# Optimization experiments

Hardware: AMD Instinct MI355X
Metric: run time of the kernel (lower is better)

Reference implementation:

```python
import jax, jax.numpy as jnp
import numpy as np

B, T, I, H, O = 8192, 1024, 7, 100, 1


def setup_inputs() -> dict:
    key = jax.random.key(0)
    ks = jax.random.split(key, 7)
    s = 1.0 / np.sqrt(H)  # PyTorch default init bound for RNN/Linear(H)
    return {
        "x": jax.random.normal(ks[0], (B, T, I), dtype=jnp.float32),
        "W_ih": jax.random.uniform(ks[1], (H, I), jnp.float32, -s, s),
        "W_hh": jax.random.uniform(ks[2], (H, H), jnp.float32, -s, s),
        "b_ih": jax.random.uniform(ks[3], (H,), jnp.float32, -s, s),
        "b_hh": jax.random.uniform(ks[4], (H,), jnp.float32, -s, s),
        "W_fc": jax.random.uniform(ks[5], (O, H), jnp.float32, -s, s),
        "b_fc": jax.random.uniform(ks[6], (O,), jnp.float32, -s, s),
    }


def reference(x, W_ih, W_hh, b_ih, b_hh, W_fc, b_fc):
    # Precompute the input projection for all timesteps in one GEMM:
    # x_proj[b,t,h] = x[b,t,:] @ W_ih^T + b_ih + b_hh  (both biases folded in)
    x_proj = jnp.einsum('bti,hi->bth', x, W_ih) + b_ih + b_hh  # [B,T,H]

    def step(h, xt):
        # h_t = relu(x_t W_ih^T + b_ih + h_{t-1} W_hh^T + b_hh)
        h_new = jax.nn.relu(xt + h @ W_hh.T)
        return h_new, None

    h0 = jnp.zeros((x.shape[0], W_hh.shape[0]), dtype=x.dtype)  # [B,H]
    hT, _ = jax.lax.scan(step, h0, jnp.swapaxes(x_proj, 0, 1))  # scan over T

    # fc applied to last timestep only: out[:, -1, :] @ W_fc^T + b_fc
    return hT @ W_fc.T + b_fc  # [B,O]
```

## Files before the change

### kernel.cpp

```cpp
#include <hip/hip_runtime.h>


typedef _Float16 half8 __attribute__((ext_vector_type(8)));
typedef float f32x4 __attribute__((ext_vector_type(4)));
typedef unsigned u32x4 __attribute__((ext_vector_type(4)));

static __device__ __forceinline__ unsigned pkrtz(float a, float b) {
    return __builtin_bit_cast(unsigned, __builtin_amdgcn_cvt_pkrtz(a, b));
}

static __device__ __forceinline__ f32x4 ld4(const float* p) {
    typedef f32x4 __attribute__((aligned(4))) f32x4a;
    return *(const f32x4a*)p;
}

__global__ __launch_bounds__(64, 1)
void rnn_wave(const float* __restrict__ x,
              const float* __restrict__ W_ih,
              const float* __restrict__ W_hh,
              const float* __restrict__ b_ih,
              const float* __restrict__ b_hh,
              const float* __restrict__ W_fc,
              const float* __restrict__ b_fc,
              float* __restrict__ out) {
    const int l  = threadIdx.x;
    const int lm = l & 15;
    const int q  = l >> 4;
    const bool q1 = (q == 1);

    half8 w[7][4];
#pragma unroll
    for (int ti = 0; ti < 7; ++ti) {
        const int np = 16 * ti + lm;
#pragma unroll
        for (int kt = 0; kt < 4; ++kt) {
            half8 hw;
#pragma unroll
            for (int jj = 0; jj < 8; ++jj) {
                float v = 0.f;
                if (np < 100) {
                    if (jj < 4) {
                        int p = 16 * kt + 4 * q + jj;
                        if (p < 100) v = W_hh[np * 100 + p];
                    } else if (kt < 3) {
                        int p = 16 * (kt + 4) + 4 * q + (jj - 4);
                        if (p < 100) v = W_hh[np * 100 + p];
                    } else {
                        if (q == 0)      v = W_ih[np * 7 + (jj - 4)];
                        else if (q == 1) v = (jj < 7) ? W_ih[np * 7 + jj]
                                             : (b_ih[np] + b_hh[np]);
                    }
                }
                hw[jj] = (_Float16)v;
            }
            w[ti][kt] = hw;
        }
    }

    const float* xr = x + (size_t)(blockIdx.x * 16 + lm) * 7168;
    const int xo = q1 ? 3 : 0;

    const u32x4 zz = {0u, 0u, 0u, 0u};
    const half8 hz = __builtin_bit_cast(half8, zz);

    half8 hf[4];
    {
        f32x4 v = ld4(xr + xo);
        float x0 = q1 ? v.y : v.x, x1 = q1 ? v.z : v.y;
        float x2 = q1 ? v.w : v.z, x3 = q1 ? 1.0f : v.w;
        hf[0] = hz; hf[1] = hz; hf[2] = hz;
        u32x4 h3 = {0u, 0u, pkrtz(x0, x1), pkrtz(x2, x3)};
        hf[3] = __builtin_bit_cast(half8, h3);
    }

    float xv[4][4];
#pragma unroll
    for (int s = 1; s <= 4; ++s) {
        f32x4 v = ld4(xr + s * 7 + xo);
        xv[s & 3][0] = q1 ? v.y : v.x;
        xv[s & 3][1] = q1 ? v.z : v.y;
        xv[s & 3][2] = q1 ? v.w : v.z;
        xv[s & 3][3] = q1 ? 1.0f : v.w;
    }

    const f32x4 kZ = {0.f, 0.f, 0.f, 0.f};
    f32x4 acc[7];

    for (int tb = 0; tb < 1024; tb += 4) {
#pragma unroll
        for (int u = 0; u < 4; ++u) {
            const int t = tb + u;

#pragma unroll
            for (int kt = 0; kt < 4; ++kt) {
                const int order[7] = {0, 4, 1, 5, 2, 6, 3};
#pragma unroll
                for (int oi = 0; oi < 7; ++oi) {
                    const int ti = order[oi];
                    acc[ti] = __builtin_amdgcn_mfma_f32_16x16x32_f16(
                        w[ti][kt], hf[kt], (kt == 0) ? kZ : acc[ti], 0, 0, 0);
                }
            }

            const int s = (u + 1) & 3;
#pragma unroll
            for (int kt = 0; kt < 3; ++kt) {
                u32x4 d;
                d.x = pkrtz(acc[kt][0],     acc[kt][1]);
                d.y = pkrtz(acc[kt][2],     acc[kt][3]);
                d.z = pkrtz(acc[kt + 4][0], acc[kt + 4][1]);
                d.w = pkrtz(acc[kt + 4][2], acc[kt + 4][3]);
                hf[kt] = __builtin_elementwise_max(__builtin_bit_cast(half8, d), hz);
            }
            {
                u32x4 d;
                d.x = pkrtz(fmaxf(acc[3][0], 0.f), fmaxf(acc[3][1], 0.f));
                d.y = pkrtz(fmaxf(acc[3][2], 0.f), fmaxf(acc[3][3], 0.f));
                d.z = pkrtz(xv[s][0], xv[s][1]);
                d.w = pkrtz(xv[s][2], xv[s][3]);
                hf[3] = __builtin_bit_cast(half8, d);
            }

            int tn = t + 5; if (tn > 1023) tn = 1023;
            {
                f32x4 v = ld4(xr + tn * 7 + xo);
                xv[s][0] = q1 ? v.y : v.x;
                xv[s][1] = q1 ? v.z : v.y;
                xv[s][2] = q1 ? v.w : v.z;
                xv[s][3] = q1 ? 1.0f : v.w;
            }
        }
    }

    float sum = 0.f;
#pragma unroll
    for (int ti = 0; ti < 7; ++ti) {
#pragma unroll
        for (int r = 0; r < 4; ++r) {
            const int np = 16 * ti + 4 * q + r;
            const float wf = (np < 100) ? W_fc[np] : 0.f;
            sum += wf * fmaxf(acc[ti][r], 0.f);
        }
    }
    sum += __shfl_xor(sum, 16, 64);
    sum += __shfl_xor(sum, 32, 64);
    if (q == 0) out[blockIdx.x * 16 + lm] = sum + b_fc[0];
}

extern "C" void kernel_launch(void* const* d_in, const int* in_sizes, int n_in,
                              void* d_out, int out_size, void* d_ws, size_t ws_size,
                              hipStream_t stream) {
    const float* x    = (const float*)d_in[0];
    const float* W_ih = (const float*)d_in[1];
    const float* W_hh = (const float*)d_in[2];
    const float* b_ih = (const float*)d_in[3];
    const float* b_hh = (const float*)d_in[4];
    const float* W_fc = (const float*)d_in[5];
    const float* b_fc = (const float*)d_in[6];
    float* out = (float*)d_out;

    rnn_wave<<<dim3(512), dim3(64), 0, stream>>>(x, W_ih, W_hh, b_ih, b_hh, W_fc, b_fc, out);
}
```

Baseline: 670.8 us.

## Interleave hidden-state packing with MFMAs using sched_group_barrier ordering

```diff
diff --git a/kernel.cpp b/kernel.cpp
--- a/kernel.cpp
+++ b/kernel.cpp
@@ -13,6 +13,8 @@
     typedef f32x4 __attribute__((aligned(4))) f32x4a;
     return *(const f32x4a*)p;
 }
+
+#define SGB(mask, n) __builtin_amdgcn_sched_group_barrier(mask, n, 0)
 
 __global__ __launch_bounds__(64, 1)
 void rnn_wave(const float* __restrict__ x,
@@ -63,72 +65,101 @@
     const u32x4 zz = {0u, 0u, 0u, 0u};
     const half8 hz = __builtin_bit_cast(half8, zz);
 
-    half8 hf[4];
-    {
-        f32x4 v = ld4(xr + xo);
-        float x0 = q1 ? v.y : v.x, x1 = q1 ? v.z : v.y;
-        float x2 = q1 ? v.w : v.z, x3 = q1 ? 1.0f : v.w;
-        hf[0] = hz; hf[1] = hz; hf[2] = hz;
-        u32x4 h3 = {0u, 0u, pkrtz(x0, x1), pkrtz(x2, x3)};
-        hf[3] = __builtin_bit_cast(half8, h3);
-    }
-
-    float xv[4][4];
+    f32x4 xv[4];
 #pragma unroll
-    for (int s = 1; s <= 4; ++s) {
-        f32x4 v = ld4(xr + s * 7 + xo);
-        xv[s & 3][0] = q1 ? v.y : v.x;
-        xv[s & 3][1] = q1 ? v.z : v.y;
-        xv[s & 3][2] = q1 ? v.w : v.z;
-        xv[s & 3][3] = q1 ? 1.0f : v.w;
-    }
+    for (int s = 0; s < 4; ++s) xv[s] = ld4(xr + s * 7 + xo);
 
     const f32x4 kZ = {0.f, 0.f, 0.f, 0.f};
     f32x4 acc[7];
+#pragma unroll
+    for (int i = 0; i < 7; ++i) acc[i] = kZ;
+    half8 hf[4];
 
     for (int tb = 0; tb < 1024; tb += 4) {
 #pragma unroll
         for (int u = 0; u < 4; ++u) {
             const int t = tb + u;
 
+            {
+                u32x4 d;
+                d.x = pkrtz(acc[0][0], acc[0][1]);
+                d.y = pkrtz(acc[0][2], acc[0][3]);
+                d.z = pkrtz(acc[4][0], acc[4][1]);
+                d.w = pkrtz(acc[4][2], acc[4][3]);
+                hf[0] = __builtin_elementwise_max(__builtin_bit_cast(half8, d), hz);
+            }
+            SGB(0x2, 8);
+            acc[0] = __builtin_amdgcn_mfma_f32_16x16x32_f16(w[0][0], hf[0], kZ, 0, 0, 0);
+            acc[4] = __builtin_amdgcn_mfma_f32_16x16x32_f16(w[4][0], hf[0], kZ, 0, 0, 0);
+            SGB(0x8, 2);
+            {
+                u32x4 d;
+                d.x = pkrtz(acc[1][0], acc[1][1]);
+                d.y = pkrtz(acc[1][2], acc[1][3]);
+                d.z = pkrtz(acc[5][0], acc[5][1]);
+                d.w = pkrtz(acc[5][2], acc[5][3]);
+                hf[1] = __builtin_elementwise_max(__builtin_bit_cast(half8, d), hz);
+            }
+            SGB(0x2, 8);
+            acc[1] = __builtin_amdgcn_mfma_f32_16x16x32_f16(w[1][0], hf[0], kZ, 0, 0, 0);
+            acc[5] = __builtin_amdgcn_mfma_f32_16x16x32_f16(w[5][0], hf[0], kZ, 0, 0, 0);
+            SGB(0x8, 2);
+            {
+                u32x4 d;
+                d.x = pkrtz(acc[2][0], acc[2][1]);
+                d.y = pkrtz(acc[2][2], acc[2][3]);
+                d.z = pkrtz(acc[6][0], acc[6][1]);
+                d.w = pkrtz(acc[6][2], acc[6][3]);
+                hf[2] = __builtin_elementwise_max(__builtin_bit_cast(half8, d), hz);
+            }
+            SGB(0x2, 8);
+            acc[2] = __builtin_amdgcn_mfma_f32_16x16x32_f16(w[2][0], hf[0], kZ, 0, 0, 0);
+            acc[6] = __builtin_amdgcn_mfma_f32_16x16x32_f16(w[6][0], hf[0], kZ, 0, 0, 0);
+            SGB(0x8, 2);
+            {
+                f32x4 v = xv[u];
+                float a_ = q1 ? v.y : v.x, b_ = q1 ? v.z : v.y;
+                float c_ = q1 ? v.w : v.z, e_ = q1 ? 1.0f : v.w;
+                u32x4 d;
+                d.x = pkrtz(fmaxf(acc[3][0], 0.f), fmaxf(acc[3][1], 0.f));
+                d.y = pkrtz(fmaxf(acc[3][2], 0.f), fmaxf(acc[3][3], 0.f));
+                d.z = pkrtz(a_, b_);
+                d.w = pkrtz(c_, e_);
+                hf[3] = __builtin_bit_cast(half8, d);
+            }
+            SGB(0x2, 12);
+            acc[3] = __builtin_amdgcn_mfma_f32_16x16x32_f16(w[3][0], hf[0], kZ, 0, 0, 0);
+            SGB(0x8, 1);
+
+            acc[0] = __builtin_amdgcn_mfma_f32_16x16x32_f16(w[0][1], hf[1], acc[0], 0, 0, 0);
+            acc[1] = __builtin_amdgcn_mfma_f32_16x16x32_f16(w[1][1], hf[1], acc[1], 0, 0, 0);
+            SGB(0x8, 2);
+            {
+                int tn = t + 4; if (tn > 1023) tn = 1023;
+                xv[u] = ld4(xr + tn * 7 + xo);
+            }
+            SGB(0x20, 1);
+            acc[2] = __builtin_amdgcn_mfma_f32_16x16x32_f16(w[2][1], hf[1], acc[2], 0, 0, 0);
+            acc[3] = __builtin_amdgcn_mfma_f32_16x16x32_f16(w[3][1], hf[1], acc[3], 0, 0, 0);
+            acc[4] = __builtin_amdgcn_mfma_f32_16x16x32_f16(w[4][1], hf[1], acc[4], 0, 0, 0);
+            acc[5] = __builtin_amdgcn_mfma_f32_16x16x32_f16(w[5][1], hf[1], acc[5], 0, 0, 0);
+            acc[6] = __builtin_amdgcn_mfma_f32_16x16x32_f16(w[6][1], hf[1], acc[6], 0, 0, 0);
+            SGB(0x8, 5);
+
 #pragma unroll
-            for (int kt = 0; kt < 4; ++kt) {
+            for (int ti = 0; ti < 7; ++ti)
+                acc[ti] = __builtin_amdgcn_mfma_f32_16x16x32_f16(w[ti][2], hf[2], acc[ti], 0, 0, 0);
+            SGB(0x8, 7);
+
+            {
                 const int order[7] = {0, 4, 1, 5, 2, 6, 3};
 #pragma unroll
                 for (int oi = 0; oi < 7; ++oi) {
                     const int ti = order[oi];
-                    acc[ti] = __builtin_amdgcn_mfma_f32_16x16x32_f16(
-                        w[ti][kt], hf[kt], (kt == 0) ? kZ : acc[ti], 0, 0, 0);
+                    acc[ti] = __builtin_amdgcn_mfma_f32_16x16x32_f16(w[ti][3], hf[3], acc[ti], 0, 0, 0);
                 }
             }
-
-            const int s = (u + 1) & 3;
-#pragma unroll
-            for (int kt = 0; kt < 3; ++kt) {
-                u32x4 d;
-                d.x = pkrtz(acc[kt][0],     acc[kt][1]);
-                d.y = pkrtz(acc[kt][2],     acc[kt][3]);
-                d.z = pkrtz(acc[kt + 4][0], acc[kt + 4][1]);
-                d.w = pkrtz(acc[kt + 4][2], acc[kt + 4][3]);
-                hf[kt] = __builtin_elementwise_max(__builtin_bit_cast(half8, d), hz);
-            }
-            {
-                u32x4 d;
-                d.x = pkrtz(fmaxf(acc[3][0], 0.f), fmaxf(acc[3][1], 0.f));
-                d.y = pkrtz(fmaxf(acc[3][2], 0.f), fmaxf(acc[3][3], 0.f));
-                d.z = pkrtz(xv[s][0], xv[s][1]);
-                d.w = pkrtz(xv[s][2], xv[s][3]);
-                hf[3] = __builtin_bit_cast(half8, d);
-            }
-
-            int tn = t + 5; if (tn > 1023) tn = 1023;
-            {
-                f32x4 v = ld4(xr + tn * 7 + xo);
-                xv[s][0] = q1 ? v.y : v.x;
-                xv[s][1] = q1 ? v.z : v.y;
-                xv[s][2] = q1 ? v.w : v.z;
-                xv[s][3] = q1 ? 1.0f : v.w;
-            }
+            SGB(0x8, 7);
         }
     }
 
```

Result: faster. 647.0 us (-3.6%).

## Split MFMA accumulation into even/odd chains and interleave packing with MFMAs

Applied to the files above, without the earlier changes.

```diff
diff --git a/kernel.cpp b/kernel.cpp
--- a/kernel.cpp
+++ b/kernel.cpp
@@ -13,6 +13,23 @@
     typedef f32x4 __attribute__((aligned(4))) f32x4a;
     return *(const f32x4a*)p;
 }
+
+static __device__ __forceinline__ half8 pack_relu(f32x4 e0, f32x4 o0,
+                                                  f32x4 e1, f32x4 o1) {
+    const u32x4 zz = {0u, 0u, 0u, 0u};
+    const half8 hz = __builtin_bit_cast(half8, zz);
+    f32x4 s0 = e0 + o0;
+    f32x4 s1 = e1 + o1;
+    u32x4 d;
+    d.x = pkrtz(s0[0], s0[1]);
+    d.y = pkrtz(s0[2], s0[3]);
+    d.z = pkrtz(s1[0], s1[1]);
+    d.w = pkrtz(s1[2], s1[3]);
+    return __builtin_elementwise_max(__builtin_bit_cast(half8, d), hz);
+}
+
+#define SGB(mask, n) __builtin_amdgcn_sched_group_barrier(mask, n, 0)
+#define MFMA16(a, b, c) __builtin_amdgcn_mfma_f32_16x16x32_f16(a, b, c, 0, 0, 0)
 
 __global__ __launch_bounds__(64, 1)
 void rnn_wave(const float* __restrict__ x,
@@ -60,75 +77,79 @@
     const float* xr = x + (size_t)(blockIdx.x * 16 + lm) * 7168;
     const int xo = q1 ? 3 : 0;
 
-    const u32x4 zz = {0u, 0u, 0u, 0u};
-    const half8 hz = __builtin_bit_cast(half8, zz);
-
-    half8 hf[4];
-    {
-        f32x4 v = ld4(xr + xo);
-        float x0 = q1 ? v.y : v.x, x1 = q1 ? v.z : v.y;
-        float x2 = q1 ? v.w : v.z, x3 = q1 ? 1.0f : v.w;
-        hf[0] = hz; hf[1] = hz; hf[2] = hz;
-        u32x4 h3 = {0u, 0u, pkrtz(x0, x1), pkrtz(x2, x3)};
-        hf[3] = __builtin_bit_cast(half8, h3);
-    }
-
-    float xv[4][4];
+    f32x4 xv[4];
 #pragma unroll
-    for (int s = 1; s <= 4; ++s) {
-        f32x4 v = ld4(xr + s * 7 + xo);
-        xv[s & 3][0] = q1 ? v.y : v.x;
-        xv[s & 3][1] = q1 ? v.z : v.y;
-        xv[s & 3][2] = q1 ? v.w : v.z;
-        xv[s & 3][3] = q1 ? 1.0f : v.w;
-    }
+    for (int s = 0; s < 4; ++s) xv[s] = ld4(xr + s * 7 + xo);
 
     const f32x4 kZ = {0.f, 0.f, 0.f, 0.f};
-    f32x4 acc[7];
+    f32x4 accE[7], accO[7];
+#pragma unroll
+    for (int i = 0; i < 7; ++i) { accE[i] = kZ; accO[i] = kZ; }
+    half8 hf[4];
 
     for (int tb = 0; tb < 1024; tb += 4) {
 #pragma unroll
         for (int u = 0; u < 4; ++u) {
             const int t = tb + u;
 
-#pragma unroll
-            for (int kt = 0; kt < 4; ++kt) {
-                const int order[7] = {0, 4, 1, 5, 2, 6, 3};
-#pragma unroll
-                for (int oi = 0; oi < 7; ++oi) {
-                    const int ti = order[oi];
-                    acc[ti] = __builtin_amdgcn_mfma_f32_16x16x32_f16(
-                        w[ti][kt], hf[kt], (kt == 0) ? kZ : acc[ti], 0, 0, 0);
-                }
-            }
+            hf[0] = pack_relu(accE[0], accO[0], accE[4], accO[4]);
+            hf[2] = pack_relu(accE[2], accO[2], accE[6], accO[6]);
+            SGB(0x2, 24);
 
-            const int s = (u + 1) & 3;
-#pragma unroll
-            for (int kt = 0; kt < 3; ++kt) {
+            accE[0] = MFMA16(w[0][0], hf[0], kZ);
+            accO[0] = MFMA16(w[0][2], hf[2], kZ);
+            accE[4] = MFMA16(w[4][0], hf[0], kZ);
+            accO[4] = MFMA16(w[4][2], hf[2], kZ);
+            SGB(0x8, 4);
+            hf[1] = pack_relu(accE[1], accO[1], accE[5], accO[5]);
+            SGB(0x2, 12);
+            accE[1] = MFMA16(w[1][0], hf[0], kZ);
+            accO[1] = MFMA16(w[1][2], hf[2], kZ);
+            accE[5] = MFMA16(w[5][0], hf[0], kZ);
+            accO[5] = MFMA16(w[5][2], hf[2], kZ);
+            SGB(0x8, 4);
+            {
+                f32x4 s3 = accE[3] + accO[3];
+                f32x4 v = xv[u];
+                float a_ = q1 ? v.y : v.x, b_ = q1 ? v.z : v.y;
+                float c_ = q1 ? v.w : v.z, e_ = q1 ? 1.0f : v.w;
                 u32x4 d;
-                d.x = pkrtz(acc[kt][0],     acc[kt][1]);
-                d.y = pkrtz(acc[kt][2],     acc[kt][3]);
-                d.z = pkrtz(acc[kt + 4][0], acc[kt + 4][1]);
-                d.w = pkrtz(acc[kt + 4][2], acc[kt + 4][3]);
-                hf[kt] = __builtin_elementwise_max(__builtin_bit_cast(half8, d), hz);
-            }
-            {
-                u32x4 d;
-                d.x = pkrtz(fmaxf(acc[3][0], 0.f), fmaxf(acc[3][1], 0.f));
-                d.y = pkrtz(fmaxf(acc[3][2], 0.f), fmaxf(acc[3][3], 0.f));
-                d.z = pkrtz(xv[s][0], xv[s][1]);
-                d.w = pkrtz(xv[s][2], xv[s][3]);
+                d.x = pkrtz(fmaxf(s3[0], 0.f), fmaxf(s3[1], 0.f));
+                d.y = pkrtz(fmaxf(s3[2], 0.f), fmaxf(s3[3], 0.f));
+                d.z = pkrtz(a_, b_);
+                d.w = pkrtz(c_, e_);
                 hf[3] = __builtin_bit_cast(half8, d);
             }
+            SGB(0x2, 14);
+            accE[2] = MFMA16(w[2][0], hf[0], kZ);
+            accO[2] = MFMA16(w[2][2], hf[2], kZ);
+            accE[6] = MFMA16(w[6][0], hf[0], kZ);
+            accO[6] = MFMA16(w[6][2], hf[2], kZ);
+            accE[3] = MFMA16(w[3][0], hf[0], kZ);
+            accO[3] = MFMA16(w[3][2], hf[2], kZ);
+            SGB(0x8, 6);
 
-            int tn = t + 5; if (tn > 1023) tn = 1023;
             {
-                f32x4 v = ld4(xr + tn * 7 + xo);
-                xv[s][0] = q1 ? v.y : v.x;
-                xv[s][1] = q1 ? v.z : v.y;
-                xv[s][2] = q1 ? v.w : v.z;
-                xv[s][3] = q1 ? 1.0f : v.w;
+                int tn = t + 4; if (tn > 1023) tn = 1023;
+                xv[u] = ld4(xr + tn * 7 + xo);
             }
+            SGB(0x20, 1);
+
+            accE[0] = MFMA16(w[0][1], hf[1], accE[0]);
+            accO[0] = MFMA16(w[0][3], hf[3], accO[0]);
+            accE[4] = MFMA16(w[4][1], hf[1], accE[4]);
+            accO[4] = MFMA16(w[4][3], hf[3], accO[4]);
+            accE[1] = MFMA16(w[1][1], hf[1], accE[1]);
+            accO[1] = MFMA16(w[1][3], hf[3], accO[1]);
+            accE[5] = MFMA16(w[5][1], hf[1], accE[5]);
+            accO[5] = MFMA16(w[5][3], hf[3], accO[5]);
+            accE[2] = MFMA16(w[2][1], hf[1], accE[2]);
+            accO[2] = MFMA16(w[2][3], hf[3], accO[2]);
+            accE[6] = MFMA16(w[6][1], hf[1], accE[6]);
+            accO[6] = MFMA16(w[6][3], hf[3], accO[6]);
+            accE[3] = MFMA16(w[3][1], hf[1], accE[3]);
+            accO[3] = MFMA16(w[3][3], hf[3], accO[3]);
+            SGB(0x8, 14);
         }
     }
 
@@ -139,7 +160,7 @@
         for (int r = 0; r < 4; ++r) {
             const int np = 16 * ti + 4 * q + r;
             const float wf = (np < 100) ? W_fc[np] : 0.f;
-            sum += wf * fmaxf(acc[ti][r], 0.f);
+            sum += wf * fmaxf(accE[ti][r] + accO[ti][r], 0.f);
         }
     }
     sum += __shfl_xor(sum, 16, 64);
```

Result: slower. 684.9 us (+2.1%).
